# Performance work log

Hardware: AMD Instinct MI355X
Metric: run time of the kernel (lower is better)

Reference implementation:

```python
import jax, jax.numpy as jnp
import numpy as np

T, B, I, H = 512, 256, 128, 256

def setup_inputs() -> dict:
    key = jax.random.key(0)
    ks = jax.random.split(key, 8)
    s_ih = 1.0 / np.sqrt(H)
    return {
        "x": jax.random.normal(ks[0], (T, B, I), dtype=jnp.float32),
        "gt": jax.random.uniform(ks[1], (T, B, 1), dtype=jnp.float32),
        "W_ih": jax.random.uniform(ks[2], (3 * H, I), minval=-s_ih, maxval=s_ih, dtype=jnp.float32),
        "W_hh": jax.random.uniform(ks[3], (3 * H, H), minval=-s_ih, maxval=s_ih, dtype=jnp.float32),
        "b_ih": jax.random.uniform(ks[4], (3 * H,), minval=-s_ih, maxval=s_ih, dtype=jnp.float32),
        "b_hh": jax.random.uniform(ks[5], (3 * H,), minval=-s_ih, maxval=s_ih, dtype=jnp.float32),
        "W_dec": jax.random.uniform(ks[6], (1, H), minval=-s_ih, maxval=s_ih, dtype=jnp.float32),
        "b_dec": jax.random.uniform(ks[7], (1,), minval=-s_ih, maxval=s_ih, dtype=jnp.float32),
    }

def reference(x, gt, W_ih, W_hh, b_ih, b_hh, W_dec, b_dec):
    h_dim = W_hh.shape[1]

    def step(h, inp):
        xt, gtt = inp  # xt: [B, I], gtt: [B, 1]
        gi = xt @ W_ih.T + b_ih          # [B, 3H]
        gh = h @ W_hh.T + b_hh           # [B, 3H]
        i_r, i_z, i_n = jnp.split(gi, 3, axis=-1)
        h_r, h_z, h_n = jnp.split(gh, 3, axis=-1)
        r = jax.nn.sigmoid(i_r + h_r)
        z = jax.nn.sigmoid(i_z + h_z)
        n = jnp.tanh(i_n + r * h_n)
        h_new = (1.0 - z) * n + z * h    # [B, H]
        logit = h_new @ W_dec.T + b_dec  # [B, 1]
        # BCE(sigmoid(logit), gt), reduction='sum': stable log-sigmoid form
        loss = -jnp.sum(gtt * jax.nn.log_sigmoid(logit)
                        + (1.0 - gtt) * jax.nn.log_sigmoid(-logit))
        return h_new, loss

    h0 = jnp.zeros((x.shape[1], h_dim), dtype=x.dtype)
    _, losses = jax.lax.scan(step, h0, (x[:-1], gt[1:]))
    return jnp.sum(losses)
```

## Files before the change

### kernel.cpp

```cpp
#include <hip/hip_runtime.h>
#include <hip/hip_bf16.h>


typedef __bf16 bf16x8_t __attribute__((ext_vector_type(8)));
typedef float floatx4_t __attribute__((ext_vector_type(4)));
typedef int intx4_t __attribute__((ext_vector_type(4)));
typedef unsigned int u32;
typedef u32 u32x4_t __attribute__((ext_vector_type(4)));

#define SW 2032.0f
#define SH 127.0f
#define INV_S (1.0f / (127.0f * 2032.0f))
#define NL2E (-1.44269504088896f)
#define CRZ (NL2E * INV_S)
#define CN (2.0f * NL2E * INV_S)

static __device__ inline u32 pack2bf(float a, float b) {
  __bf16 x = (__bf16)a, y = (__bf16)b;
  unsigned short ux = *(unsigned short*)&x, uy = *(unsigned short*)&y;
  return (u32)ux | ((u32)uy << 16);
}

__global__ void prep_kernel(const float* __restrict__ Whh,
                            const float* __restrict__ Wdec,
                            const float* __restrict__ Wih,
                            char* __restrict__ Wq, char* __restrict__ wdq,
                            __bf16* __restrict__ Wihb,
                            float* __restrict__ h_ws, float* __restrict__ out) {
  int idx = blockIdx.x * 256 + threadIdx.x;
  for (int i = idx; i < 768 * 256; i += 65536) {
    int v = (int)rintf(Whh[i] * SW);
    v = v > 127 ? 127 : (v < -127 ? -127 : v);
    Wq[i] = (char)v;
  }
  for (int i = idx; i < 768 * 128; i += 65536) Wihb[i] = (__bf16)Wih[i];
  if (idx < 256) {
    int v = (int)rintf(Wdec[idx] * SW);
    v = v > 127 ? 127 : (v < -127 ? -127 : v);
    wdq[idx] = (char)v;
  }
  if (idx < 65536) h_ws[idx] = 0.f;
  if (idx == 0) out[0] = 0.f;
}

__global__ __launch_bounds__(256) void xconv_kernel(const float* __restrict__ x,
                                                    __bf16* __restrict__ xb) {
  const size_t i = ((size_t)blockIdx.x * 256 + threadIdx.x) * 8;
  floatx4_t a = *(const floatx4_t*)(x + i);
  floatx4_t b = *(const floatx4_t*)(x + i + 4);
  bf16x8_t t;
#pragma unroll
  for (int j = 0; j < 4; ++j) {
    t[j] = (__bf16)a[j];
    t[4 + j] = (__bf16)b[j];
  }
  *(bf16x8_t*)(xb + i) = t;
}

__global__ __launch_bounds__(256) void gemm1_kernel(
    const __bf16* __restrict__ xb,
    const __bf16* __restrict__ Wihb,
    const float* __restrict__ bih, const float* __restrict__ bhh,
    u32* __restrict__ giw) {
  __shared__ __bf16 As[128][144];
  __shared__ __bf16 Bs[128][144];

  const int tid = threadIdx.x;
  const int w = tid >> 6, lane = tid & 63;
  const int q = lane >> 4, nh = lane & 15;
  const int n0 = blockIdx.x * 128;
  const int b0 = blockIdx.y * 128;
  const int wm = w >> 1, wn = w & 1;

  {
    const bf16x8_t* sa = (const bf16x8_t*)(Wihb + (size_t)n0 * 128);
    const bf16x8_t* sb = (const bf16x8_t*)(xb + (size_t)b0 * 128);
    const int rr = tid >> 4, cc = (tid & 15) * 8;
#pragma unroll
    for (int v = 0; v < 8; ++v) {
      *(bf16x8_t*)&As[v * 16 + rr][cc] = sa[v * 256 + tid];
      *(bf16x8_t*)&Bs[v * 16 + rr][cc] = sb[v * 256 + tid];
    }
  }
  __syncthreads();

  floatx4_t acc[4][4];
#pragma unroll
  for (int a = 0; a < 4; ++a)
#pragma unroll
    for (int b = 0; b < 4; ++b)
#pragma unroll
      for (int j = 0; j < 4; ++j) acc[a][b][j] = 0.f;

#pragma unroll
  for (int kk = 0; kk < 4; ++kk) {
    bf16x8_t af[4], bf[4];
#pragma unroll
    for (int mt = 0; mt < 4; ++mt)
      af[mt] = *(const bf16x8_t*)&As[wm * 64 + mt * 16 + nh][kk * 32 + q * 8];
#pragma unroll
    for (int nt = 0; nt < 4; ++nt)
      bf[nt] = *(const bf16x8_t*)&Bs[wn * 64 + nt * 16 + nh][kk * 32 + q * 8];
#pragma unroll
    for (int mt = 0; mt < 4; ++mt)
#pragma unroll
      for (int nt = 0; nt < 4; ++nt)
        acc[mt][nt] = __builtin_amdgcn_mfma_f32_16x16x32_bf16(
            af[mt], bf[nt], acc[mt][nt], 0, 0, 0);
  }

  const int gate = n0 >> 8;
  const float sc = (gate < 2) ? NL2E : (2.0f * NL2E);
  const int wr_base = ((n0 & 255) >> 5) + wm * 2;
#pragma unroll
  for (int a = 0; a < 2; ++a) {
    const int nnA = n0 + wm * 64 + a * 32 + q * 4;
    floatx4_t biasA = *(const floatx4_t*)(bih + nnA);
    floatx4_t biasB = *(const floatx4_t*)(bih + nnA + 16);
    if (gate < 2) {
      floatx4_t c1 = *(const floatx4_t*)(bhh + nnA);
      floatx4_t c2 = *(const floatx4_t*)(bhh + nnA + 16);
#pragma unroll
      for (int j = 0; j < 4; ++j) {
        biasA[j] += c1[j];
        biasB[j] += c2[j];
      }
    }
    const int wrec = wr_base + a;
#pragma unroll
    for (int nt = 0; nt < 4; ++nt) {
      const int bb = b0 + wn * 64 + nt * 16 + nh;
      const int tl = bb >> 8, gg = (bb >> 2) & 63, jb = bb & 3;
      size_t U =
          (((size_t)tl * 64 + gg) * 3 + gate) * 512 + wrec * 64 + jb * 16 + q * 4;
      u32x4_t pv;
#pragma unroll
      for (int j = 0; j < 4; ++j)
        pv[j] = pack2bf((acc[2 * a][nt][j] + biasA[j]) * sc,
                        (acc[2 * a + 1][nt][j] + biasB[j]) * sc);
      *(u32x4_t*)(giw + U) = pv;
    }
  }
}

__global__ __launch_bounds__(512, 2) void rec_kernel(
    const char* __restrict__ Wq,
    const char* __restrict__ wdq,
    const u32* __restrict__ gi,
    const float* __restrict__ gt, const float* __restrict__ bdec,
    const float* __restrict__ bhh, float* __restrict__ h_ws,
    float* __restrict__ out, int t0, int tc) {
  __shared__ char hb[2][4][288];
  __shared__ float logitbuf[2048];

  const int tid = threadIdx.x;
  const int w = tid >> 6, lane = tid & 63;
  const int q = lane >> 4, nh = lane & 15;
  const int g = blockIdx.x;
  const int col0 = w * 32 + nh;
  const int col1 = col0 + 16;

  intx4_t wf[6][4];
#pragma unroll
  for (int c = 0; c < 3; ++c)
#pragma unroll
    for (int ss = 0; ss < 2; ++ss) {
      const int n = c * 256 + w * 32 + ss * 16 + nh;
#pragma unroll
      for (int kb = 0; kb < 4; ++kb)
        wf[c * 2 + ss][kb] =
            *(const intx4_t*)(Wq + (size_t)n * 256 + kb * 64 + q * 16);
    }
  intx4_t wdf[4];
#pragma unroll
  for (int kb = 0; kb < 4; ++kb) {
    intx4_t z = {0, 0, 0, 0};
    intx4_t v = *(const intx4_t*)(wdq + kb * 64 + q * 16);
    wdf[kb] = (nh == 0) ? v : z;
  }

  const float bn20 = 2.0f * NL2E * bhh[512 + col0];
  const float bn21 = 2.0f * NL2E * bhh[512 + col1];
  const float bdec0 = bdec[0];

  if (tid < 256) {
    const int rr = tid >> 6, c0 = (tid & 63) * 4;
    u32 p = 0;
#pragma unroll
    for (int j = 0; j < 4; ++j) {
      int a = (int)rintf(h_ws[(size_t)(g * 4 + rr) * 256 + c0 + j] * SH);
      a = a > 127 ? 127 : (a < -127 ? -127 : a);
      p |= ((u32)(a & 255)) << (8 * j);
    }
    *(u32*)&hb[0][rr][c0] = p;
  }
  float ho0 = h_ws[(size_t)(g * 4 + q) * 256 + col0];
  float ho1 = h_ws[(size_t)(g * 4 + q) * 256 + col1];
  __syncthreads();

  const int tcm1 = tc - 1;
  u32 GA[3], GB[3];
  {
    size_t u0 = ((size_t)g * 3) * 512 + w * 64 + lane;
#pragma unroll
    for (int c = 0; c < 3; ++c) GA[c] = gi[u0 + c * 512];
    const int t1 = tc > 1 ? 1 : 0;
    size_t u1 = (((size_t)t1 * 64 + g) * 3) * 512 + w * 64 + lane;
#pragma unroll
    for (int c = 0; c < 3; ++c) GB[c] = gi[u1 + c * 512];
  }

  auto STEP = [&](int T, u32* G, int TPRE) {
    const int pb = T & 1;
    intx4_t hbf[4];
#pragma unroll
    for (int kb = 0; kb < 4; ++kb)
      hbf[kb] = *(const intx4_t*)&hb[pb][nh >> 2][kb * 64 + q * 16];

    const float gr0 = __uint_as_float(G[0] << 16);
    const float gr1 = __uint_as_float(G[0] & 0xffff0000u);
    const float gz0 = __uint_as_float(G[1] << 16);
    const float gz1 = __uint_as_float(G[1] & 0xffff0000u);
    const float an0 = __uint_as_float(G[2] << 16);
    const float an1 = __uint_as_float(G[2] & 0xffff0000u);
    {
      size_t up = (((size_t)TPRE * 64 + g) * 3) * 512 + w * 64 + lane;
#pragma unroll
      for (int c = 0; c < 3; ++c) G[c] = gi[up + c * 512];
    }

    intx4_t acc[6], facc;
#pragma unroll
    for (int cs = 0; cs < 6; ++cs)
#pragma unroll
      for (int jj = 0; jj < 4; ++jj) acc[cs][jj] = 0;
#pragma unroll
    for (int jj = 0; jj < 4; ++jj) facc[jj] = 0;

#pragma unroll
    for (int kb = 0; kb < 4; ++kb) {
#pragma unroll
      for (int cs = 0; cs < 6; ++cs)
        acc[cs] = __builtin_amdgcn_mfma_i32_16x16x64_i8(hbf[kb], wf[cs][kb],
                                                        acc[cs], 0, 0, 0);
      if (w == 0)
        facc = __builtin_amdgcn_mfma_i32_16x16x64_i8(hbf[kb], wdf[kb], facc,
                                                     0, 0, 0);
    }

    float rr0 = __builtin_amdgcn_rcpf(
        1.f + __builtin_amdgcn_exp2f((float)acc[0][0] * CRZ + gr0));
    float rr1 = __builtin_amdgcn_rcpf(
        1.f + __builtin_amdgcn_exp2f((float)acc[1][0] * CRZ + gr1));
    float zz0 = __builtin_amdgcn_rcpf(
        1.f + __builtin_amdgcn_exp2f((float)acc[2][0] * CRZ + gz0));
    float zz1 = __builtin_amdgcn_rcpf(
        1.f + __builtin_amdgcn_exp2f((float)acc[3][0] * CRZ + gz1));
    float hn20 = (float)acc[4][0] * CN + bn20;
    float hn21 = (float)acc[5][0] * CN + bn21;
    float tv0 = 2.f * __builtin_amdgcn_rcpf(
                          1.f + __builtin_amdgcn_exp2f(rr0 * hn20 + an0)) -
                1.f;
    float tv1 = 2.f * __builtin_amdgcn_rcpf(
                          1.f + __builtin_amdgcn_exp2f(rr1 * hn21 + an1)) -
                1.f;
    float hnew0 = tv0 + zz0 * (ho0 - tv0);
    float hnew1 = tv1 + zz1 * (ho1 - tv1);
    ho0 = hnew0;
    ho1 = hnew1;
    int h0 = (int)rintf(hnew0 * SH);
    int h1 = (int)rintf(hnew1 * SH);
    hb[1 - pb][q][col0] = (char)h0;
    hb[1 - pb][q][col1] = (char)h1;

    if (w == 0 && nh == 0 && T >= 1)
      logitbuf[(T - 1) * 4 + q] = (float)facc[0] * INV_S + bdec0;

    asm volatile("s_waitcnt lgkmcnt(0)" ::: "memory");
    __builtin_amdgcn_s_barrier();
    asm volatile("" ::: "memory");
  };

  int t = 0;
#pragma unroll 1
  for (; t + 1 < tc; t += 2) {
    STEP(t, GA, (t + 2 <= tcm1) ? t + 2 : tcm1);
    STEP(t + 1, GB, (t + 3 <= tcm1) ? t + 3 : tcm1);
  }
  if (t < tc) STEP(t, GA, tcm1);

  if (w == 0) {
    intx4_t fac2 = {0, 0, 0, 0};
#pragma unroll
    for (int kb = 0; kb < 4; ++kb) {
      intx4_t b = *(const intx4_t*)&hb[tc & 1][nh >> 2][kb * 64 + q * 16];
      fac2 = __builtin_amdgcn_mfma_i32_16x16x64_i8(b, wdf[kb], fac2, 0, 0, 0);
    }
    if (nh == 0) logitbuf[(tc - 1) * 4 + q] = (float)fac2[0] * INV_S + bdec0;
  }
  __syncthreads();

  float loss = 0.f;
  for (int i = tid; i < tc * 4; i += 512) {
    float l = logitbuf[i];
    float gtv = gt[(size_t)(t0 + (i >> 2) + 1) * 256 + g * 4 + (i & 3)];
    float t1 = log1pf(__expf(-fabsf(l)));
    loss += gtv * (fmaxf(-l, 0.f) + t1) + (1.f - gtv) * (fmaxf(l, 0.f) + t1);
  }
  loss += __shfl_xor(loss, 1);
  loss += __shfl_xor(loss, 2);
  loss += __shfl_xor(loss, 4);
  loss += __shfl_xor(loss, 8);
  loss += __shfl_xor(loss, 16);
  loss += __shfl_xor(loss, 32);
  if (lane == 0) atomicAdd(out, loss);

  h_ws[(size_t)(g * 4 + q) * 256 + col0] = ho0;
  h_ws[(size_t)(g * 4 + q) * 256 + col1] = ho1;
}

extern "C" void kernel_launch(void* const* d_in, const int* in_sizes, int n_in,
                              void* d_out, int out_size, void* d_ws,
                              size_t ws_size, hipStream_t stream) {
  const float* x = (const float*)d_in[0];
  const float* gt = (const float*)d_in[1];
  const float* Wih = (const float*)d_in[2];
  const float* Whh = (const float*)d_in[3];
  const float* bih = (const float*)d_in[4];
  const float* bhh = (const float*)d_in[5];
  const float* Wdec = (const float*)d_in[6];
  const float* bdec = (const float*)d_in[7];
  float* out = (float*)d_out;

  char* ws = (char*)d_ws;
  char* Wq = ws;
  char* wdq = ws + 196608;
  float* h_ws = (float*)(ws + 197120);
  __bf16* Wihb = (__bf16*)(ws + 459264);
  char* dyn = ws + 655872;
  const size_t per_step = (size_t)393216 + 65536;
  size_t avail = ws_size > 655872 ? ws_size - 655872 : per_step;
  int Tc = (int)(avail / per_step);
  if (Tc < 1) Tc = 1;
  if (Tc > 511) Tc = 511;
  __bf16* xb = (__bf16*)dyn;
  u32* gi = (u32*)(dyn + (size_t)Tc * 65536);

  prep_kernel<<<256, 256, 0, stream>>>(Whh, Wdec, Wih, Wq, wdq, Wihb, h_ws,
                                       out);
  for (int t0 = 0; t0 < 511; t0 += Tc) {
    const int tc = (511 - t0 < Tc) ? (511 - t0) : Tc;
    xconv_kernel<<<tc * 16, 256, 0, stream>>>(x + (size_t)t0 * 256 * 128, xb);
    gemm1_kernel<<<dim3(6, tc * 2), 256, 0, stream>>>(xb, Wihb, bih, bhh, gi);
    rec_kernel<<<64, 512, 0, stream>>>(Wq, wdq, gi, gt, bdec, bhh, h_ws, out,
                                       t0, tc);
  }
}
```

Before: 518.6 us.

## Double recurrent block to 1024 threads, halving per-wave columns and splitting decoder MFMA

The recurrent kernel now runs 16 waves per block instead of 8, so each wave owns 16 hidden columns (3 MFMA chains instead of 6) and keeps half the weight fragments in registers. The decoder logit dot product, previously four serial MFMAs on wave 0, is split across waves 12-15 with one MFMA each; the partial sums go to shared memory and are added in the loss phase. This shortens the per-step critical path in the serial recurrence, at the cost of a barrier across more waves each step and more shared memory for the partial logits.

```diff
diff --git a/kernel.cpp b/kernel.cpp
--- a/kernel.cpp
+++ b/kernel.cpp
@@ -143,7 +143,7 @@
   }
 }
 
-__global__ __launch_bounds__(512, 2) void rec_kernel(
+__global__ __launch_bounds__(1024) void rec_kernel(
     const char* __restrict__ Wq,
     const char* __restrict__ wdq,
     const u32* __restrict__ gi,
@@ -151,36 +151,33 @@
     const float* __restrict__ bhh, float* __restrict__ h_ws,
     float* __restrict__ out, int t0, int tc) {
   __shared__ char hb[2][4][288];
-  __shared__ float logitbuf[2048];
+  __shared__ float lp[4][2048];
 
   const int tid = threadIdx.x;
   const int w = tid >> 6, lane = tid & 63;
   const int q = lane >> 4, nh = lane & 15;
   const int g = blockIdx.x;
-  const int col0 = w * 32 + nh;
-  const int col1 = col0 + 16;
-
-  intx4_t wf[6][4];
-#pragma unroll
-  for (int c = 0; c < 3; ++c)
-#pragma unroll
-    for (int ss = 0; ss < 2; ++ss) {
-      const int n = c * 256 + w * 32 + ss * 16 + nh;
-#pragma unroll
-      for (int kb = 0; kb < 4; ++kb)
-        wf[c * 2 + ss][kb] =
-            *(const intx4_t*)(Wq + (size_t)n * 256 + kb * 64 + q * 16);
-    }
-  intx4_t wdf[4];
-#pragma unroll
-  for (int kb = 0; kb < 4; ++kb) {
+  const int col = w * 16 + nh;
+  const int wp = w >> 1;
+  const int hi = w & 1;
+
+  intx4_t wf[3][4];
+#pragma unroll
+  for (int c = 0; c < 3; ++c) {
+    const int n = c * 256 + col;
+#pragma unroll
+    for (int kb = 0; kb < 4; ++kb)
+      wf[c][kb] = *(const intx4_t*)(Wq + (size_t)n * 256 + kb * 64 + q * 16);
+  }
+  intx4_t wdfk;
+  {
+    const int kb = (w >= 12) ? (w - 12) : 0;
     intx4_t z = {0, 0, 0, 0};
     intx4_t v = *(const intx4_t*)(wdq + kb * 64 + q * 16);
-    wdf[kb] = (nh == 0) ? v : z;
-  }
-
-  const float bn20 = 2.0f * NL2E * bhh[512 + col0];
-  const float bn21 = 2.0f * NL2E * bhh[512 + col1];
+    wdfk = (nh == 0) ? v : z;
+  }
+
+  const float bn2 = 2.0f * NL2E * bhh[512 + col];
   const float bdec0 = bdec[0];
 
   if (tid < 256) {
@@ -194,18 +191,18 @@
     }
     *(u32*)&hb[0][rr][c0] = p;
   }
-  float ho0 = h_ws[(size_t)(g * 4 + q) * 256 + col0];
-  float ho1 = h_ws[(size_t)(g * 4 + q) * 256 + col1];
+  float ho = h_ws[(size_t)(g * 4 + q) * 256 + col];
   __syncthreads();
 
   const int tcm1 = tc - 1;
+  const size_t boff = (size_t)wp * 64 + q * 16 + nh;
   u32 GA[3], GB[3];
   {
-    size_t u0 = ((size_t)g * 3) * 512 + w * 64 + lane;
+    size_t u0 = ((size_t)g * 3) * 512 + boff;
 #pragma unroll
     for (int c = 0; c < 3; ++c) GA[c] = gi[u0 + c * 512];
-    const int t1 = tc > 1 ? 1 : 0;
-    size_t u1 = (((size_t)t1 * 64 + g) * 3) * 512 + w * 64 + lane;
+    const int t1s = tc > 1 ? 1 : 0;
+    size_t u1 = (((size_t)t1s * 64 + g) * 3) * 512 + boff;
 #pragma unroll
     for (int c = 0; c < 3; ++c) GB[c] = gi[u1 + c * 512];
   }
@@ -217,64 +214,56 @@
     for (int kb = 0; kb < 4; ++kb)
       hbf[kb] = *(const intx4_t*)&hb[pb][nh >> 2][kb * 64 + q * 16];
 
-    const float gr0 = __uint_as_float(G[0] << 16);
-    const float gr1 = __uint_as_float(G[0] & 0xffff0000u);
-    const float gz0 = __uint_as_float(G[1] << 16);
-    const float gz1 = __uint_as_float(G[1] & 0xffff0000u);
-    const float an0 = __uint_as_float(G[2] << 16);
-    const float an1 = __uint_as_float(G[2] & 0xffff0000u);
+    float gv0, gv1, gv2;
+    if (hi) {
+      gv0 = __uint_as_float(G[0] & 0xffff0000u);
+      gv1 = __uint_as_float(G[1] & 0xffff0000u);
+      gv2 = __uint_as_float(G[2] & 0xffff0000u);
+    } else {
+      gv0 = __uint_as_float(G[0] << 16);
+      gv1 = __uint_as_float(G[1] << 16);
+      gv2 = __uint_as_float(G[2] << 16);
+    }
     {
-      size_t up = (((size_t)TPRE * 64 + g) * 3) * 512 + w * 64 + lane;
+      size_t up = (((size_t)TPRE * 64 + g) * 3) * 512 + boff;
 #pragma unroll
       for (int c = 0; c < 3; ++c) G[c] = gi[up + c * 512];
     }
 
-    intx4_t acc[6], facc;
-#pragma unroll
-    for (int cs = 0; cs < 6; ++cs)
+    intx4_t acc[3];
+#pragma unroll
+    for (int cs = 0; cs < 3; ++cs)
 #pragma unroll
       for (int jj = 0; jj < 4; ++jj) acc[cs][jj] = 0;
-#pragma unroll
-    for (int jj = 0; jj < 4; ++jj) facc[jj] = 0;
-
-#pragma unroll
-    for (int kb = 0; kb < 4; ++kb) {
-#pragma unroll
-      for (int cs = 0; cs < 6; ++cs)
+
+#pragma unroll
+    for (int kb = 0; kb < 4; ++kb)
+#pragma unroll
+      for (int cs = 0; cs < 3; ++cs)
         acc[cs] = __builtin_amdgcn_mfma_i32_16x16x64_i8(hbf[kb], wf[cs][kb],
                                                         acc[cs], 0, 0, 0);
-      if (w == 0)
-        facc = __builtin_amdgcn_mfma_i32_16x16x64_i8(hbf[kb], wdf[kb], facc,
-                                                     0, 0, 0);
+
+    if (w >= 12) {
+      intx4_t hsel = (w == 12) ? hbf[0]
+                   : (w == 13) ? hbf[1]
+                   : (w == 14) ? hbf[2] : hbf[3];
+      intx4_t facc = {0, 0, 0, 0};
+      facc = __builtin_amdgcn_mfma_i32_16x16x64_i8(hsel, wdfk, facc, 0, 0, 0);
+      if (nh == 0 && T >= 1) lp[w - 12][(T - 1) * 4 + q] = (float)facc[0];
     }
 
     float rr0 = __builtin_amdgcn_rcpf(
-        1.f + __builtin_amdgcn_exp2f((float)acc[0][0] * CRZ + gr0));
-    float rr1 = __builtin_amdgcn_rcpf(
-        1.f + __builtin_amdgcn_exp2f((float)acc[1][0] * CRZ + gr1));
+        1.f + __builtin_amdgcn_exp2f((float)acc[0][0] * CRZ + gv0));
     float zz0 = __builtin_amdgcn_rcpf(
-        1.f + __builtin_amdgcn_exp2f((float)acc[2][0] * CRZ + gz0));
-    float zz1 = __builtin_amdgcn_rcpf(
-        1.f + __builtin_amdgcn_exp2f((float)acc[3][0] * CRZ + gz1));
-    float hn20 = (float)acc[4][0] * CN + bn20;
-    float hn21 = (float)acc[5][0] * CN + bn21;
+        1.f + __builtin_amdgcn_exp2f((float)acc[1][0] * CRZ + gv1));
+    float hn2 = (float)acc[2][0] * CN + bn2;
     float tv0 = 2.f * __builtin_amdgcn_rcpf(
-                          1.f + __builtin_amdgcn_exp2f(rr0 * hn20 + an0)) -
+                          1.f + __builtin_amdgcn_exp2f(rr0 * hn2 + gv2)) -
                 1.f;
-    float tv1 = 2.f * __builtin_amdgcn_rcpf(
-                          1.f + __builtin_amdgcn_exp2f(rr1 * hn21 + an1)) -
-                1.f;
-    float hnew0 = tv0 + zz0 * (ho0 - tv0);
-    float hnew1 = tv1 + zz1 * (ho1 - tv1);
-    ho0 = hnew0;
-    ho1 = hnew1;
-    int h0 = (int)rintf(hnew0 * SH);
-    int h1 = (int)rintf(hnew1 * SH);
-    hb[1 - pb][q][col0] = (char)h0;
-    hb[1 - pb][q][col1] = (char)h1;
-
-    if (w == 0 && nh == 0 && T >= 1)
-      logitbuf[(T - 1) * 4 + q] = (float)facc[0] * INV_S + bdec0;
+    float hnew = tv0 + zz0 * (ho - tv0);
+    ho = hnew;
+    int h8 = (int)rintf(hnew * SH);
+    hb[1 - pb][q][col] = (char)h8;
 
     asm volatile("s_waitcnt lgkmcnt(0)" ::: "memory");
     __builtin_amdgcn_s_barrier();
@@ -289,20 +278,18 @@
   }
   if (t < tc) STEP(t, GA, tcm1);
 
-  if (w == 0) {
+  if (w >= 12) {
+    const int kb = w - 12;
+    intx4_t b = *(const intx4_t*)&hb[tc & 1][nh >> 2][kb * 64 + q * 16];
     intx4_t fac2 = {0, 0, 0, 0};
-#pragma unroll
-    for (int kb = 0; kb < 4; ++kb) {
-      intx4_t b = *(const intx4_t*)&hb[tc & 1][nh >> 2][kb * 64 + q * 16];
-      fac2 = __builtin_amdgcn_mfma_i32_16x16x64_i8(b, wdf[kb], fac2, 0, 0, 0);
-    }
-    if (nh == 0) logitbuf[(tc - 1) * 4 + q] = (float)fac2[0] * INV_S + bdec0;
+    fac2 = __builtin_amdgcn_mfma_i32_16x16x64_i8(b, wdfk, fac2, 0, 0, 0);
+    if (nh == 0) lp[kb][(tc - 1) * 4 + q] = (float)fac2[0];
   }
   __syncthreads();
 
   float loss = 0.f;
-  for (int i = tid; i < tc * 4; i += 512) {
-    float l = logitbuf[i];
+  for (int i = tid; i < tc * 4; i += 1024) {
+    float l = (lp[0][i] + lp[1][i] + lp[2][i] + lp[3][i]) * INV_S + bdec0;
     float gtv = gt[(size_t)(t0 + (i >> 2) + 1) * 256 + g * 4 + (i & 3)];
     float t1 = log1pf(__expf(-fabsf(l)));
     loss += gtv * (fmaxf(-l, 0.f) + t1) + (1.f - gtv) * (fmaxf(l, 0.f) + t1);
@@ -315,8 +302,7 @@
   loss += __shfl_xor(loss, 32);
   if (lane == 0) atomicAdd(out, loss);
 
-  h_ws[(size_t)(g * 4 + q) * 256 + col0] = ho0;
-  h_ws[(size_t)(g * 4 + q) * 256 + col1] = ho1;
+  h_ws[(size_t)(g * 4 + q) * 256 + col] = ho;
 }
 
 extern "C" void kernel_launch(void* const* d_in, const int* in_sizes, int n_in,
@@ -352,7 +338,7 @@
     const int tc = (511 - t0 < Tc) ? (511 - t0) : Tc;
     xconv_kernel<<<tc * 16, 256, 0, stream>>>(x + (size_t)t0 * 256 * 128, xb);
     gemm1_kernel<<<dim3(6, tc * 2), 256, 0, stream>>>(xb, Wihb, bih, bhh, gi);
-    rec_kernel<<<64, 512, 0, stream>>>(Wq, wdq, gi, gt, bdec, bhh, h_ws, out,
-                                       t0, tc);
-  }
-}
+    rec_kernel<<<64, 1024, 0, stream>>>(Wq, wdq, gi, gt, bdec, bhh, h_ws, out,
+                                        t0, tc);
+  }
+}
```

Result: no change. 518.0 us (-0.1%).
